# Kernel tuning notes

Hardware: AMD Instinct MI355X
Metric: run time of the kernel (lower is better)

Reference implementation:

```python
import jax, jax.numpy as jnp
import numpy as np

N, E, B = 65536, 262144, 2048   # nodes, edges, graphs
ND, ED, H, L = 32, 8, 128, 4    # node feat, edge feat, hidden, egnn layers
PE, PH, CH = 1280, 512, 512     # protein embed, protein hidden, combined hidden
EPS = 1e-8


def _seg_mean(data, ids, num):
    s = jax.ops.segment_sum(data, ids, num_segments=num)
    c = jax.ops.segment_sum(jnp.ones((data.shape[0], 1), data.dtype), ids, num_segments=num)
    return s / jnp.clip(c, 1.0)


def setup_inputs() -> dict:
    key = jax.random.key(0)
    ks = iter(jax.random.split(key, 40))

    def p(shape, scale=0.05):
        return jax.random.normal(next(ks), shape, dtype=jnp.float32) * scale

    inp = {
        "x": jax.random.normal(next(ks), (N, ND), dtype=jnp.float32),
        "pos": jax.random.normal(next(ks), (N, 3), dtype=jnp.float32),
        "edge_attr": jax.random.uniform(next(ks), (E, ED), dtype=jnp.float32),
        "protein_embedding": jax.random.normal(next(ks), (B, PE), dtype=jnp.float32),
        "edge_index": jax.random.randint(next(ks), (2, E), 0, N),
        "batch": jnp.arange(N, dtype=jnp.int64) // (N // B),
        # EGNN embeddings
        "emb_in_w": p((ND, H)), "emb_in_b": p((H,)),
        "emb_out_w": p((H, H)), "emb_out_b": p((H,)),
        # per-layer stacked params (leading dim L)
        "edge_w1": p((L, 2 * H + 1 + ED, H)), "edge_b1": p((L, H)),
        "edge_w2": p((L, H, H)), "edge_b2": p((L, H)),
        "att_w": p((L, H, 1)), "att_b": p((L, 1)),
        "coord_w1": p((L, H, H)), "coord_b1": p((L, H)),
        "coord_w2": p((L, H, 1)),  # no bias, xavier in torch impl
        "node_w1": p((L, 2 * H, H)), "node_b1": p((L, H)),
        "node_w2": p((L, H, H)), "node_b2": p((L, H)),
        # protein + combined heads
        "prot_w": p((PE, PH)), "prot_b": p((PH,)),
        "comb_w1": p((H + PH, CH)), "comb_b1": p((CH,)),
        "comb_w2": p((CH, 1)), "comb_b2": p((1,)),
    }
    return inp


def _forward(x, pos, edge_attr, protein_embedding,
             emb_in_w, emb_in_b, emb_out_w, emb_out_b,
             edge_w1, edge_b1, edge_w2, edge_b2, att_w, att_b,
             coord_w1, coord_b1, coord_w2,
             node_w1, node_b1, node_w2, node_b2,
             prot_w, prot_b, comb_w1, comb_b1, comb_w2, comb_b2,
             edge_index, batch):
    row, col = edge_index[0], edge_index[1]
    h = x @ emb_in_w + emb_in_b
    for l in range(L):
        # coord2radial (normalize=True)
        d = pos[row] - pos[col]                       # [E,3]
        radial = jnp.sum(d * d, axis=-1, keepdims=True)  # [E,1]
        d = d / (jnp.sqrt(radial) + EPS)
        # edge model with sigmoid attention gate
        e_in = jnp.concatenate([h[row], h[col], radial, edge_attr], axis=-1)
        m = jax.nn.silu(e_in @ edge_w1[l] + edge_b1[l])
        m = jax.nn.silu(m @ edge_w2[l] + edge_b2[l])
        m = m * jax.nn.sigmoid(m @ att_w[l] + att_b[l])
        # coord model (tanh=True, coords_agg='mean')
        t = jax.nn.silu(m @ coord_w1[l] + coord_b1[l])
        trans = d * jnp.tanh(t @ coord_w2[l])         # [E,3]
        pos = pos + _seg_mean(trans, row, N)
        # node model (sum aggregation, residual)
        agg = jax.ops.segment_sum(m, row, num_segments=N)
        nh = jax.nn.silu(jnp.concatenate([h, agg], axis=-1) @ node_w1[l] + node_b1[l])
        h = h + (nh @ node_w2[l] + node_b2[l])
    h = h @ emb_out_w + emb_out_b
    # global mean pool over graphs
    drug = _seg_mean(h, batch, B)                     # [B,H]
    prot = jax.nn.relu(protein_embedding @ prot_w + prot_b)  # dropout = identity (eval)
    c = jnp.concatenate([drug, prot], axis=-1)
    c = jax.nn.relu(c @ comb_w1 + comb_b1)
    logits = (c @ comb_w2 + comb_b2)[:, 0]
    return logits


def reference(x, pos, edge_attr, protein_embedding,
              emb_in_w, emb_in_b, emb_out_w, emb_out_b,
              edge_w1, edge_b1, edge_w2, edge_b2, att_w, att_b,
              coord_w1, coord_b1, coord_w2,
              node_w1, node_b1, node_w2, node_b2,
              prot_w, prot_b, comb_w1, comb_b1, comb_w2, comb_b2,
              edge_index, batch):
    logits = _forward(x, pos, edge_attr, protein_embedding,
                      emb_in_w, emb_in_b, emb_out_w, emb_out_b,
                      edge_w1, edge_b1, edge_w2, edge_b2, att_w, att_b,
                      coord_w1, coord_b1, coord_w2,
                      node_w1, node_b1, node_w2, node_b2,
                      prot_w, prot_b, comb_w1, comb_b1, comb_w2, comb_b2,
                      edge_index, batch)
    attention_weights = jnp.zeros((B, 1, 1), dtype=logits.dtype)
    return logits, attention_weights
```

## Files before the change

### kernel.cpp

```cpp
#include <hip/hip_runtime.h>
#include <math.h>


static constexpr int NN  = 65536;
static constexpr int NE  = 262144;
static constexpr int NB  = 2048;
static constexpr int NDF = 32;
static constexpr int HD  = 128;
static constexpr int NL  = 4;
static constexpr int PED = 1280;
static constexpr int PHD = 512;
static constexpr int CHD = 512;
static constexpr float EPSV = 1e-8f;

static constexpr int KK1 = 9;
static constexpr int KK2 = 4;
static constexpr int KKN1 = 8;
static constexpr int KKP = 40;
static constexpr int KKC = 20;

static constexpr int ES = 36;

typedef __attribute__((ext_vector_type(8))) short bf8_t;
typedef __attribute__((ext_vector_type(4))) float f4_t;

__device__ __forceinline__ float sigmoid_f(float x) {
  return __fdividef(1.0f, 1.0f + __expf(-x));
}
__device__ __forceinline__ float silu_f(float x) { return x * sigmoid_f(x); }

__device__ __forceinline__ ushort f2bf(float f) {
  unsigned u = __float_as_uint(f);
  u += 0x7FFFu + ((u >> 16) & 1u);
  return (ushort)(u >> 16);
}
__device__ __forceinline__ float bf2f(ushort h) {
  return __uint_as_float(((unsigned)h) << 16);
}
__device__ __forceinline__ unsigned pk2bf(float a, float b) {
  return (unsigned)f2bf(a) | ((unsigned)f2bf(b) << 16);
}

__device__ __forceinline__ void fma44(float (&acc)[4][4], const float4 a, const float4 w) {
  const float av[4] = {a.x, a.y, a.z, a.w};
  const float wv[4] = {w.x, w.y, w.z, w.w};
#pragma unroll
  for (int i = 0; i < 4; ++i)
#pragma unroll
    for (int j = 0; j < 4; ++j) acc[i][j] = fmaf(av[i], wv[j], acc[i][j]);
}


__global__ void hist_kernel(const int* __restrict__ ei, int* __restrict__ deg) {
  const int e = blockIdx.x * 256 + threadIdx.x;
  if (e < NE) atomicAdd(&deg[ei[e]], 1);
}

__global__ __launch_bounds__(1024) void scan_kernel(const int* __restrict__ deg,
                                                    int* __restrict__ row_ptr) {
  __shared__ int wsums[16];
  __shared__ int carry_s;
  const int t = threadIdx.x;
  const int lane = t & 63, wave = t >> 6;
  if (t == 0) { carry_s = 0; row_ptr[0] = 0; }
  __syncthreads();
  for (int c = 0; c < NN / 1024; ++c) {
    const int i = c * 1024 + t;
    int incl = deg[i];
#pragma unroll
    for (int d = 1; d < 64; d <<= 1) {
      const int u = __shfl_up(incl, d, 64);
      if (lane >= d) incl += u;
    }
    if (lane == 63) wsums[wave] = incl;
    __syncthreads();
    if (t == 0) {
      int a = carry_s;
#pragma unroll
      for (int w = 0; w < 16; ++w) { const int tmp = wsums[w]; wsums[w] = a; a += tmp; }
      carry_s = a;
    }
    __syncthreads();
    row_ptr[i + 1] = wsums[wave] + incl;
    __syncthreads();
  }
}

__global__ void fill_kernel(const int* __restrict__ ei, const int* __restrict__ row_ptr,
                            int* __restrict__ fill_pos, int* __restrict__ edge_ids) {
  const int e = blockIdx.x * 256 + threadIdx.x;
  if (e < NE) {
    const int n = ei[e];
    const int s = atomicAdd(&fill_pos[n], 1);
    edge_ids[row_ptr[n] + s] = e;
  }
}

__global__ void perm_kernel(const int* __restrict__ ei, const int* __restrict__ edge_ids,
                            const float* __restrict__ edge_attr,
                            int* __restrict__ rowp, int* __restrict__ colp,
                            float* __restrict__ eap) {
  const int i = blockIdx.x * 256 + threadIdx.x;
  if (i >= NE) return;
  const int e = edge_ids[i];
  rowp[i] = ei[e];
  colp[i] = ei[NE + e];
  const float4 a = *(const float4*)(edge_attr + (size_t)e * 8);
  const float4 b = *(const float4*)(edge_attr + (size_t)e * 8 + 4);
  *(float4*)(eap + (size_t)i * 8) = a;
  *(float4*)(eap + (size_t)i * 8 + 4) = b;
}

__global__ void pos_copy_kernel(const float* __restrict__ pos, float* __restrict__ pc) {
  const int n = blockIdx.x * 256 + threadIdx.x;
  if (n < NN) {
    const float4 v = make_float4(pos[(size_t)n * 3 + 0], pos[(size_t)n * 3 + 1],
                                 pos[(size_t)n * 3 + 2], 0.0f);
    *(float4*)(pc + (size_t)n * 4) = v;
  }
}


__global__ __launch_bounds__(256) void packw_kernel(
    const float* __restrict__ W, ushort* __restrict__ Wp,
    int K, int N, int KK, size_t sW, size_t sWp) {
  const int layer = blockIdx.y;
  const int NTG = N >> 4;
  const int i = blockIdx.x * 256 + threadIdx.x;
  if (i >= KK * NTG * 64) return;
  const int l = i & 63;
  const int q = i >> 6;
  const int ntg = q % NTG;
  const int kk = q / NTG;
  const int k0 = kk * 32 + ((l >> 4) * 8);
  const int n = ntg * 16 + (l & 15);
  const float* w = W + layer * sW;
  unsigned ww[4];
#pragma unroll
  for (int p = 0; p < 4; ++p) {
    const int ka = k0 + p * 2, kb = ka + 1;
    const unsigned lo = (ka < K) ? f2bf(w[(size_t)ka * N + n]) : 0;
    const unsigned hi = (kb < K) ? f2bf(w[(size_t)kb * N + n]) : 0;
    ww[p] = lo | (hi << 16);
  }
  *(uint4*)(Wp + layer * sWp + (size_t)i * 8) = make_uint4(ww[0], ww[1], ww[2], ww[3]);
}

__global__ __launch_bounds__(256) void cvt_bf_kernel(const float* __restrict__ in,
                                                     ushort* __restrict__ out, int n) {
  const int i = blockIdx.x * 256 + threadIdx.x;
  if (i * 8 >= n) return;
  const float4 v0 = *(const float4*)(in + (size_t)i * 8);
  const float4 v1 = *(const float4*)(in + (size_t)i * 8 + 4);
  *(uint4*)(out + (size_t)i * 8) =
      make_uint4(pk2bf(v0.x, v0.y), pk2bf(v0.z, v0.w), pk2bf(v1.x, v1.y), pk2bf(v1.z, v1.w));
}


__global__ __launch_bounds__(256) void geom_kernel(
    const float* __restrict__ pos_cur, const float* __restrict__ eap,
    const int* __restrict__ rowp, const int* __restrict__ colp,
    float* __restrict__ dnb, ushort* __restrict__ extra) {
  const int i = blockIdx.x * 256 + threadIdx.x;
  if (i >= NE) return;
  const int r = rowp[i], c = colp[i];
  const float4 pr = *(const float4*)(pos_cur + (size_t)r * 4);
  const float4 pc = *(const float4*)(pos_cur + (size_t)c * 4);
  const float dx = pr.x - pc.x, dy = pr.y - pc.y, dz = pr.z - pc.z;
  const float radial = dx * dx + dy * dy + dz * dz;
  const float inv = 1.0f / (sqrtf(radial) + EPSV);
  *(float4*)(dnb + (size_t)i * 4) = make_float4(dx * inv, dy * inv, dz * inv, 0.0f);
  const float4 ea0 = *(const float4*)(eap + (size_t)i * 8);
  const float4 ea1 = *(const float4*)(eap + (size_t)i * 8 + 4);
  ushort* dst = extra + (size_t)i * 32;
  *(uint4*)(dst) = make_uint4(pk2bf(radial, ea0.x), pk2bf(ea0.y, ea0.z),
                              pk2bf(ea0.w, ea1.x), pk2bf(ea1.y, ea1.z));
  *(uint4*)(dst + 8)  = make_uint4((unsigned)f2bf(ea1.w), 0, 0, 0);
  *(uint4*)(dst + 16) = make_uint4(0, 0, 0, 0);
  *(uint4*)(dst + 24) = make_uint4(0, 0, 0, 0);
}


__global__ __launch_bounds__(256) void emb_in_kernel(
    const float* __restrict__ x, const float* __restrict__ W,
    const float* __restrict__ B, float* __restrict__ h, ushort* __restrict__ hbf) {
  __shared__ float xs[NDF * ES];
  const int t = threadIdx.x;
  const int n0 = blockIdx.x * 32;
  {
    const int r = t >> 3;
    const int kq = (t & 7) * 4;
    const float4 v = *(const float4*)(x + (size_t)(n0 + r) * NDF + kq);
    xs[(kq + 0) * ES + r] = v.x;
    xs[(kq + 1) * ES + r] = v.y;
    xs[(kq + 2) * ES + r] = v.z;
    xs[(kq + 3) * ES + r] = v.w;
  }
  __syncthreads();
  const int eg = t & 7, fg = t >> 3;
  float acc[4][4] = {};
  const float* wp = W + fg * 4;
#pragma unroll
  for (int k = 0; k < NDF; ++k) {
    const float4 a = *(const float4*)&xs[k * ES + eg * 4];
    const float4 w = *(const float4*)(wp + (size_t)k * HD);
    fma44(acc, a, w);
  }
  const float4 bv = *(const float4*)(B + fg * 4);
  const float bb[4] = {bv.x, bv.y, bv.z, bv.w};
#pragma unroll
  for (int i = 0; i < 4; ++i) {
    const float4 o = make_float4(acc[i][0] + bb[0], acc[i][1] + bb[1],
                                 acc[i][2] + bb[2], acc[i][3] + bb[3]);
    *(float4*)(h + (size_t)(n0 + eg * 4 + i) * HD + fg * 4) = o;
    *(uint2*)(hbf + (size_t)(n0 + eg * 4 + i) * HD + fg * 4) =
        make_uint2(pk2bf(o.x, o.y), pk2bf(o.z, o.w));
  }
}


__global__ __launch_bounds__(256) void edge_mfma_kernel(
    const ushort* __restrict__ hbf, const ushort* __restrict__ extra,
    const int* __restrict__ rowp, const int* __restrict__ colp,
    const float* __restrict__ dnb,
    const ushort* __restrict__ W1p, const float* __restrict__ B1,
    const ushort* __restrict__ W2p, const float* __restrict__ B2,
    const float* __restrict__ AW, const float* __restrict__ AB,
    const ushort* __restrict__ CW1p, const float* __restrict__ CB1,
    const float* __restrict__ CW2,
    ushort* __restrict__ m_bf, float* __restrict__ trans_out) {
  __shared__ ushort mtileT[64 * 128];
  __shared__ int ridx[64], cidx[64];
  __shared__ float redbuf[2][64];
  __shared__ float gates[64];

  const int t = threadIdx.x;
  const int e0 = blockIdx.x * 64;
  if (t < 64) {
    ridx[t] = rowp[e0 + t];
    cidx[t] = colp[e0 + t];
  }
  __syncthreads();

  const int w = t >> 6, l = t & 63;
  const int wn = w & 1, we = w >> 1;
  const int g = l >> 4, ln = l & 15;
  const int nb = wn * 64;
  const int eb = we * 32;

  int je[2], er[2], ec[2], swz[2];
#pragma unroll
  for (int et = 0; et < 2; ++et) {
    je[et] = eb + et * 16 + ln;
    er[et] = ridx[je[et]];
    ec[et] = cidx[je[et]];
    swz[et] = (je[et] & 7) << 3;
  }

  const f4_t zf = {0.0f, 0.0f, 0.0f, 0.0f};
  f4_t acc[4][2];
#pragma unroll
  for (int mt = 0; mt < 4; ++mt)
#pragma unroll
    for (int et = 0; et < 2; ++et) acc[mt][et] = zf;

#pragma unroll
  for (int kk = 0; kk < KK1; ++kk) {
    bf8_t aw[4], be[2];
#pragma unroll
    for (int mt = 0; mt < 4; ++mt)
      aw[mt] = *(const bf8_t*)(W1p + ((size_t)(kk * 8 + wn * 4 + mt) * 64 + l) * 8);
#pragma unroll
    for (int et = 0; et < 2; ++et) {
      if (kk < 8) {
        const int idx = (kk < 4) ? er[et] : ec[et];
        be[et] = *(const bf8_t*)(hbf + (size_t)idx * HD + (kk & 3) * 32 + g * 8);
      } else {
        be[et] = *(const bf8_t*)(extra + (size_t)(e0 + je[et]) * 32 + g * 8);
      }
    }
#pragma unroll
    for (int mt = 0; mt < 4; ++mt)
#pragma unroll
      for (int et = 0; et < 2; ++et)
        acc[mt][et] = __builtin_amdgcn_mfma_f32_16x16x32_bf16(aw[mt], be[et], acc[mt][et], 0, 0, 0);
  }

  {
#pragma unroll
    for (int mt = 0; mt < 4; ++mt) {
      const int n0 = nb + mt * 16 + g * 4;
      const float4 bv = *(const float4*)(B1 + n0);
#pragma unroll
      for (int et = 0; et < 2; ++et) {
        const unsigned lo = pk2bf(silu_f(acc[mt][et][0] + bv.x), silu_f(acc[mt][et][1] + bv.y));
        const unsigned hi = pk2bf(silu_f(acc[mt][et][2] + bv.z), silu_f(acc[mt][et][3] + bv.w));
        *(uint2*)&mtileT[je[et] * HD + (n0 ^ swz[et])] = make_uint2(lo, hi);
      }
    }
  }
  __syncthreads();

  f4_t acc2[4][2];
#pragma unroll
  for (int mt = 0; mt < 4; ++mt)
#pragma unroll
    for (int et = 0; et < 2; ++et) acc2[mt][et] = zf;
#pragma unroll
  for (int kk = 0; kk < KK2; ++kk) {
    bf8_t aw[4], be[2];
#pragma unroll
    for (int mt = 0; mt < 4; ++mt)
      aw[mt] = *(const bf8_t*)(W2p + ((size_t)(kk * 8 + wn * 4 + mt) * 64 + l) * 8);
    const int nk = kk * 32 + g * 8;
#pragma unroll
    for (int et = 0; et < 2; ++et)
      be[et] = *(const bf8_t*)&mtileT[je[et] * HD + (nk ^ swz[et])];
#pragma unroll
    for (int mt = 0; mt < 4; ++mt)
#pragma unroll
      for (int et = 0; et < 2; ++et)
        acc2[mt][et] = __builtin_amdgcn_mfma_f32_16x16x32_bf16(aw[mt], be[et], acc2[mt][et], 0, 0, 0);
  }

  float m2v[4][2][4];
  {
    float p[2] = {0.0f, 0.0f};
#pragma unroll
    for (int mt = 0; mt < 4; ++mt) {
      const int n0 = nb + mt * 16 + g * 4;
      const float4 bv = *(const float4*)(B2 + n0);
      const float4 av = *(const float4*)(AW + n0);
      const float bb[4] = {bv.x, bv.y, bv.z, bv.w};
      const float aa[4] = {av.x, av.y, av.z, av.w};
#pragma unroll
      for (int et = 0; et < 2; ++et)
#pragma unroll
        for (int r = 0; r < 4; ++r) {
          const float v = silu_f(acc2[mt][et][r] + bb[r]);
          m2v[mt][et][r] = v;
          p[et] = fmaf(v, aa[r], p[et]);
        }
    }
#pragma unroll
    for (int et = 0; et < 2; ++et) {
      p[et] += __shfl_xor(p[et], 16, 64);
      p[et] += __shfl_xor(p[et], 32, 64);
    }
    if (l < 16) {
#pragma unroll
      for (int et = 0; et < 2; ++et) redbuf[wn][eb + et * 16 + l] = p[et];
    }
  }
  __syncthreads();
  if (t < 64) gates[t] = sigmoid_f(redbuf[0][t] + redbuf[1][t] + AB[0]);
  __syncthreads();

  {
    float grow[2];
#pragma unroll
    for (int et = 0; et < 2; ++et) grow[et] = gates[je[et]];
#pragma unroll
    for (int mt = 0; mt < 4; ++mt) {
      const int n0 = nb + mt * 16 + g * 4;
#pragma unroll
      for (int et = 0; et < 2; ++et) {
        const unsigned lo = pk2bf(m2v[mt][et][0] * grow[et], m2v[mt][et][1] * grow[et]);
        const unsigned hi = pk2bf(m2v[mt][et][2] * grow[et], m2v[mt][et][3] * grow[et]);
        *(uint2*)&mtileT[je[et] * HD + (n0 ^ swz[et])] = make_uint2(lo, hi);
      }
    }
  }
  __syncthreads();

  f4_t acc3[4][2];
#pragma unroll
  for (int mt = 0; mt < 4; ++mt)
#pragma unroll
    for (int et = 0; et < 2; ++et) acc3[mt][et] = zf;
#pragma unroll
  for (int kk = 0; kk < KK2; ++kk) {
    bf8_t aw[4], be[2];
#pragma unroll
    for (int mt = 0; mt < 4; ++mt)
      aw[mt] = *(const bf8_t*)(CW1p + ((size_t)(kk * 8 + wn * 4 + mt) * 64 + l) * 8);
    const int nk = kk * 32 + g * 8;
#pragma unroll
    for (int et = 0; et < 2; ++et)
      be[et] = *(const bf8_t*)&mtileT[je[et] * HD + (nk ^ swz[et])];
#pragma unroll
    for (int mt = 0; mt < 4; ++mt)
#pragma unroll
      for (int et = 0; et < 2; ++et)
        acc3[mt][et] = __builtin_amdgcn_mfma_f32_16x16x32_bf16(aw[mt], be[et], acc3[mt][et], 0, 0, 0);
  }
  {
    float q[2] = {0.0f, 0.0f};
#pragma unroll
    for (int mt = 0; mt < 4; ++mt) {
      const int n0 = nb + mt * 16 + g * 4;
      const float4 bv = *(const float4*)(CB1 + n0);
      const float4 cv = *(const float4*)(CW2 + n0);
      const float bb[4] = {bv.x, bv.y, bv.z, bv.w};
      const float cc[4] = {cv.x, cv.y, cv.z, cv.w};
#pragma unroll
      for (int et = 0; et < 2; ++et)
#pragma unroll
        for (int r = 0; r < 4; ++r)
          q[et] = fmaf(silu_f(acc3[mt][et][r] + bb[r]), cc[r], q[et]);
    }
#pragma unroll
    for (int et = 0; et < 2; ++et) {
      q[et] += __shfl_xor(q[et], 16, 64);
      q[et] += __shfl_xor(q[et], 32, 64);
    }
    if (l < 16) {
#pragma unroll
      for (int et = 0; et < 2; ++et) redbuf[wn][eb + et * 16 + l] = q[et];
    }
  }
  __syncthreads();
  if (t < 64) {
    const float s = tanhf(redbuf[0][t] + redbuf[1][t]);
    const f4_t dn = *(const f4_t*)(dnb + (size_t)(e0 + t) * 4);
    const f4_t tr = dn * s;
    *(f4_t*)(trans_out + (size_t)(e0 + t) * 4) = tr;
  }

#pragma unroll
  for (int it = 0; it < 4; ++it) {
    const int i = it * 256 + t;
    const int row = i >> 4;
    const int c8 = (i & 15) * 8;
    const uint4 v = *(const uint4*)&mtileT[row * HD + (c8 ^ ((row & 7) << 3))];
    *(uint4*)(m_bf + (size_t)(e0 + row) * HD + c8) = v;
  }
}


__global__ __launch_bounds__(256) void gather_kernel(
    const ushort* __restrict__ m_bf, const float* __restrict__ trans,
    const int* __restrict__ row_ptr,
    ushort* __restrict__ agg_bf, float* __restrict__ pos_cur) {
  const int t = threadIdx.x;
  const int wave = t >> 6, lane = t & 63;
  const int n = blockIdx.x * 4 + wave;
  const int s = row_ptr[n], e_end = row_ptr[n + 1];
  float a0 = 0.0f, a1 = 0.0f, ta = 0.0f;
  for (int i = s; i < e_end; ++i) {
    const ushort2 v = *(const ushort2*)(m_bf + (size_t)i * HD + lane * 2);
    a0 += bf2f(v.x);
    a1 += bf2f(v.y);
    if (lane < 4) ta += trans[(size_t)i * 4 + lane];
  }
  ushort2 ab;
  ab.x = f2bf(a0);
  ab.y = f2bf(a1);
  *(ushort2*)(agg_bf + (size_t)n * HD + lane * 2) = ab;
  if (lane < 3) {
    const int dg = e_end - s;
    pos_cur[(size_t)n * 4 + lane] += ta / (float)(dg > 0 ? dg : 1);
  }
}


__global__ __launch_bounds__(256) void node_mfma_kernel(
    float* __restrict__ h, const ushort* __restrict__ hbf,
    const ushort* __restrict__ agg_bf,
    const ushort* __restrict__ W1p, const float* __restrict__ B1,
    const ushort* __restrict__ W2p, const float* __restrict__ B2,
    ushort* __restrict__ hbf_out) {
  __shared__ ushort mtileT[64 * 128];
  const int t = threadIdx.x;
  const int n0blk = blockIdx.x * 64;
  const int w = t >> 6, l = t & 63;
  const int wn = w & 1, we = w >> 1;
  const int g = l >> 4, ln = l & 15;
  const int nb = wn * 64;
  const int eb = we * 32;

  int jn[2], swz[2];
#pragma unroll
  for (int et = 0; et < 2; ++et) {
    jn[et] = eb + et * 16 + ln;
    swz[et] = (jn[et] & 7) << 3;
  }

  const f4_t zf = {0.0f, 0.0f, 0.0f, 0.0f};
  f4_t acc[4][2];
#pragma unroll
  for (int mt = 0; mt < 4; ++mt)
#pragma unroll
    for (int et = 0; et < 2; ++et) acc[mt][et] = zf;

#pragma unroll
  for (int kk = 0; kk < KKN1; ++kk) {
    bf8_t aw[4], be[2];
#pragma unroll
    for (int mt = 0; mt < 4; ++mt)
      aw[mt] = *(const bf8_t*)(W1p + ((size_t)(kk * 8 + wn * 4 + mt) * 64 + l) * 8);
#pragma unroll
    for (int et = 0; et < 2; ++et) {
      const size_t base = (size_t)(n0blk + jn[et]) * HD + (kk & 3) * 32 + g * 8;
      be[et] = (kk < 4) ? *(const bf8_t*)(hbf + base) : *(const bf8_t*)(agg_bf + base);
    }
#pragma unroll
    for (int mt = 0; mt < 4; ++mt)
#pragma unroll
      for (int et = 0; et < 2; ++et)
        acc[mt][et] = __builtin_amdgcn_mfma_f32_16x16x32_bf16(aw[mt], be[et], acc[mt][et], 0, 0, 0);
  }
  {
#pragma unroll
    for (int mt = 0; mt < 4; ++mt) {
      const int n0 = nb + mt * 16 + g * 4;
      const float4 bv = *(const float4*)(B1 + n0);
#pragma unroll
      for (int et = 0; et < 2; ++et) {
        const unsigned lo = pk2bf(silu_f(acc[mt][et][0] + bv.x), silu_f(acc[mt][et][1] + bv.y));
        const unsigned hi = pk2bf(silu_f(acc[mt][et][2] + bv.z), silu_f(acc[mt][et][3] + bv.w));
        *(uint2*)&mtileT[jn[et] * HD + (n0 ^ swz[et])] = make_uint2(lo, hi);
      }
    }
  }
  __syncthreads();

  f4_t acc2[4][2];
#pragma unroll
  for (int mt = 0; mt < 4; ++mt)
#pragma unroll
    for (int et = 0; et < 2; ++et) acc2[mt][et] = zf;
#pragma unroll
  for (int kk = 0; kk < KK2; ++kk) {
    bf8_t aw[4], be[2];
#pragma unroll
    for (int mt = 0; mt < 4; ++mt)
      aw[mt] = *(const bf8_t*)(W2p + ((size_t)(kk * 8 + wn * 4 + mt) * 64 + l) * 8);
    const int nk = kk * 32 + g * 8;
#pragma unroll
    for (int et = 0; et < 2; ++et)
      be[et] = *(const bf8_t*)&mtileT[jn[et] * HD + (nk ^ swz[et])];
#pragma unroll
    for (int mt = 0; mt < 4; ++mt)
#pragma unroll
      for (int et = 0; et < 2; ++et)
        acc2[mt][et] = __builtin_amdgcn_mfma_f32_16x16x32_bf16(aw[mt], be[et], acc2[mt][et], 0, 0, 0);
  }
  {
#pragma unroll
    for (int mt = 0; mt < 4; ++mt) {
      const int n0 = nb + mt * 16 + g * 4;
      const float4 bv = *(const float4*)(B2 + n0);
#pragma unroll
      for (int et = 0; et < 2; ++et) {
        float* hp = h + (size_t)(n0blk + jn[et]) * HD + n0;
        const float4 old = *(const float4*)hp;
        float4 o;
        o.x = old.x + acc2[mt][et][0] + bv.x;
        o.y = old.y + acc2[mt][et][1] + bv.y;
        o.z = old.z + acc2[mt][et][2] + bv.z;
        o.w = old.w + acc2[mt][et][3] + bv.w;
        *(float4*)hp = o;
        *(uint2*)(hbf_out + (size_t)(n0blk + jn[et]) * HD + n0) =
            make_uint2(pk2bf(o.x, o.y), pk2bf(o.z, o.w));
      }
    }
  }
}


__global__ __launch_bounds__(256) void gemm_head_kernel(
    const ushort* __restrict__ A, const ushort* __restrict__ Wp,
    const float* __restrict__ bias, ushort* __restrict__ out,
    int lda, int KK, int NTG, int ldo, int col_off) {
  const int t = threadIdx.x;
  const int rb = blockIdx.x * 64;
  const int cb = blockIdx.y * 128;
  const int w = t >> 6, l = t & 63;
  const int wr = w >> 1, wc = w & 1;
  const int g = l >> 4, ln = l & 15;
  const int row0 = wr * 32;
  int rowA[2];
#pragma unroll
  for (int mt = 0; mt < 2; ++mt) rowA[mt] = row0 + mt * 16 + ln;

  const f4_t zf = {0.0f, 0.0f, 0.0f, 0.0f};
  f4_t acc[2][4];
#pragma unroll
  for (int mt = 0; mt < 2; ++mt)
#pragma unroll
    for (int nt = 0; nt < 4; ++nt) acc[mt][nt] = zf;

  const int ntg0 = (cb >> 4) + wc * 4;
  for (int kk = 0; kk < KK; ++kk) {
    bf8_t a[2], b[4];
#pragma unroll
    for (int mt = 0; mt < 2; ++mt)
      a[mt] = *(const bf8_t*)(A + (size_t)(rb + rowA[mt]) * lda + kk * 32 + g * 8);
#pragma unroll
    for (int nt = 0; nt < 4; ++nt)
      b[nt] = *(const bf8_t*)(Wp + ((size_t)(kk * NTG + ntg0 + nt) * 64 + l) * 8);
#pragma unroll
    for (int mt = 0; mt < 2; ++mt)
#pragma unroll
      for (int nt = 0; nt < 4; ++nt)
        acc[mt][nt] = __builtin_amdgcn_mfma_f32_16x16x32_bf16(a[mt], b[nt], acc[mt][nt], 0, 0, 0);
  }
  {
    float bn[4];
#pragma unroll
    for (int nt = 0; nt < 4; ++nt) bn[nt] = bias[cb + wc * 64 + nt * 16 + ln];
#pragma unroll
    for (int mt = 0; mt < 2; ++mt)
#pragma unroll
      for (int nt = 0; nt < 4; ++nt) {
        const int col = cb + wc * 64 + nt * 16 + ln;
#pragma unroll
        for (int r = 0; r < 4; ++r) {
          const int row = row0 + mt * 16 + g * 4 + r;
          const float v = fmaxf(acc[mt][nt][r] + bn[nt], 0.0f);
          out[(size_t)(rb + row) * ldo + col_off + col] = f2bf(v);
        }
      }
  }
}


__global__ __launch_bounds__(128) void pool_kernel(
    const float* __restrict__ h, const float* __restrict__ W,
    const float* __restrict__ B, ushort* __restrict__ c_in) {
  __shared__ float mh[HD];
  const int g = blockIdx.x, t = threadIdx.x;
  float s = 0.0f;
#pragma unroll 4
  for (int n = 0; n < 32; ++n) s += h[((size_t)g * 32 + n) * HD + t];
  mh[t] = s * (1.0f / 32.0f);
  __syncthreads();
  float acc = B[t];
#pragma unroll 4
  for (int k = 0; k < HD; ++k) acc = fmaf(mh[k], W[(size_t)k * HD + t], acc);
  c_in[(size_t)g * (HD + PHD) + t] = f2bf(acc);
}

__global__ __launch_bounds__(256) void logits_kernel(
    const ushort* __restrict__ c, const float* __restrict__ w2,
    const float* __restrict__ b2, float* __restrict__ out) {
  const int t = threadIdx.x;
  const int wave = t >> 6, lane = t & 63;
  const int r = blockIdx.x * 4 + wave;
  const ushort* cp = c + (size_t)r * CHD + lane * 8;
  const float* wp = w2 + lane * 8;
  float s = 0.0f;
#pragma unroll
  for (int j = 0; j < 8; ++j) s = fmaf(bf2f(cp[j]), wp[j], s);
#pragma unroll
  for (int off = 32; off > 0; off >>= 1) s += __shfl_down(s, off, 64);
  if (lane == 0) {
    out[r] = s + b2[0];
    out[NB + r] = 0.0f;
  }
}


extern "C" void kernel_launch(void* const* d_in, const int* in_sizes, int n_in,
                              void* d_out, int out_size, void* d_ws, size_t ws_size,
                              hipStream_t stream) {
  const float* x          = (const float*)d_in[0];
  const float* pos        = (const float*)d_in[1];
  const float* edge_attr  = (const float*)d_in[2];
  const float* pe         = (const float*)d_in[3];
  const int*   edge_index = (const int*)d_in[4];
  const float* emb_in_w   = (const float*)d_in[6];
  const float* emb_in_b   = (const float*)d_in[7];
  const float* emb_out_w  = (const float*)d_in[8];
  const float* emb_out_b  = (const float*)d_in[9];
  const float* edge_w1    = (const float*)d_in[10];
  const float* edge_b1    = (const float*)d_in[11];
  const float* edge_w2    = (const float*)d_in[12];
  const float* edge_b2    = (const float*)d_in[13];
  const float* att_w      = (const float*)d_in[14];
  const float* att_b      = (const float*)d_in[15];
  const float* coord_w1   = (const float*)d_in[16];
  const float* coord_b1   = (const float*)d_in[17];
  const float* coord_w2   = (const float*)d_in[18];
  const float* node_w1    = (const float*)d_in[19];
  const float* node_b1    = (const float*)d_in[20];
  const float* node_w2    = (const float*)d_in[21];
  const float* node_b2    = (const float*)d_in[22];
  const float* prot_w     = (const float*)d_in[23];
  const float* prot_b     = (const float*)d_in[24];
  const float* comb_w1    = (const float*)d_in[25];
  const float* comb_b1    = (const float*)d_in[26];
  const float* comb_w2    = (const float*)d_in[27];
  const float* comb_b2    = (const float*)d_in[28];
  float* out = (float*)d_out;
  (void)in_sizes; (void)n_in; (void)out_size; (void)ws_size;

  char* ws = (char*)d_ws;
  size_t off = 0;
  auto carve = [&](size_t bytes) -> void* {
    void* p = ws + off;
    off += (bytes + 255) & ~(size_t)255;
    return p;
  };
  float*  h       = (float*)carve((size_t)NN * HD * 4);
  ushort* h_bf    = (ushort*)carve((size_t)NN * HD * 2);
  ushort* agg_bf  = (ushort*)carve((size_t)NN * HD * 2);
  ushort* m_bf    = (ushort*)carve((size_t)NE * HD * 2);
  float*  trans   = (float*)carve((size_t)NE * 4 * 4);
  float*  dnb     = (float*)carve((size_t)NE * 4 * 4);
  ushort* extra   = (ushort*)carve((size_t)NE * 32 * 2);
  float*  eap     = (float*)carve((size_t)NE * 8 * 4);
  float*  pos_cur = (float*)carve((size_t)NN * 4 * 4);
  ushort* pe_bf   = (ushort*)carve((size_t)NB * PED * 2);
  ushort* c_in    = (ushort*)carve((size_t)NB * (HD + PHD) * 2);
  ushort* c1      = (ushort*)carve((size_t)NB * CHD * 2);
  const size_t sW1p  = (size_t)KK1 * 8 * 64 * 8;
  const size_t sW2p  = (size_t)KK2 * 8 * 64 * 8;
  const size_t sNW1p = (size_t)KKN1 * 8 * 64 * 8;
  const size_t sPWp  = (size_t)KKP * 32 * 64 * 8;
  const size_t sCWp  = (size_t)KKC * 32 * 64 * 8;
  ushort* W1p     = (ushort*)carve(sW1p * NL * 2);
  ushort* W2p     = (ushort*)carve(sW2p * NL * 2);
  ushort* CW1p    = (ushort*)carve(sW2p * NL * 2);
  ushort* NW1p    = (ushort*)carve(sNW1p * NL * 2);
  ushort* NW2p    = (ushort*)carve(sW2p * NL * 2);
  ushort* PWp     = (ushort*)carve(sPWp * 2);
  ushort* CWp     = (ushort*)carve(sCWp * 2);
  int* deg        = (int*)carve((size_t)NN * 4);
  int* row_ptr    = (int*)carve((size_t)(NN + 1) * 4);
  int* fill_pos   = (int*)carve((size_t)NN * 4);
  int* edge_ids   = (int*)carve((size_t)NE * 4);
  int* rowp       = (int*)carve((size_t)NE * 4);
  int* colp       = (int*)carve((size_t)NE * 4);

  hipMemsetAsync(deg, 0, (size_t)NN * 4, stream);
  hipMemsetAsync(fill_pos, 0, (size_t)NN * 4, stream);

  pos_copy_kernel<<<NN / 256, 256, 0, stream>>>(pos, pos_cur);
  hist_kernel<<<NE / 256, 256, 0, stream>>>(edge_index, deg);
  scan_kernel<<<1, 1024, 0, stream>>>(deg, row_ptr);
  fill_kernel<<<NE / 256, 256, 0, stream>>>(edge_index, row_ptr, fill_pos, edge_ids);
  perm_kernel<<<NE / 256, 256, 0, stream>>>(edge_index, edge_ids, edge_attr,
                                            rowp, colp, eap);

  packw_kernel<<<dim3(18, NL), 256, 0, stream>>>(edge_w1, W1p, 265, HD, KK1,
                                                 (size_t)265 * HD, sW1p);
  packw_kernel<<<dim3(8, NL), 256, 0, stream>>>(edge_w2, W2p, HD, HD, KK2,
                                                (size_t)HD * HD, sW2p);
  packw_kernel<<<dim3(8, NL), 256, 0, stream>>>(coord_w1, CW1p, HD, HD, KK2,
                                                (size_t)HD * HD, sW2p);
  packw_kernel<<<dim3(16, NL), 256, 0, stream>>>(node_w1, NW1p, 2 * HD, HD, KKN1,
                                                 (size_t)2 * HD * HD, sNW1p);
  packw_kernel<<<dim3(8, NL), 256, 0, stream>>>(node_w2, NW2p, HD, HD, KK2,
                                                (size_t)HD * HD, sW2p);
  packw_kernel<<<dim3(320, 1), 256, 0, stream>>>(prot_w, PWp, PED, PHD, KKP, 0, 0);
  packw_kernel<<<dim3(160, 1), 256, 0, stream>>>(comb_w1, CWp, HD + PHD, CHD, KKC, 0, 0);

  cvt_bf_kernel<<<NB * PED / (256 * 8), 256, 0, stream>>>(pe, pe_bf, NB * PED);

  emb_in_kernel<<<NN / 32, 256, 0, stream>>>(x, emb_in_w, emb_in_b, h, h_bf);

  for (int l = 0; l < NL; ++l) {
    geom_kernel<<<NE / 256, 256, 0, stream>>>(pos_cur, eap, rowp, colp, dnb, extra);
    edge_mfma_kernel<<<NE / 64, 256, 0, stream>>>(
        h_bf, extra, rowp, colp, dnb,
        W1p + (size_t)l * sW1p, edge_b1 + (size_t)l * HD,
        W2p + (size_t)l * sW2p, edge_b2 + (size_t)l * HD,
        att_w + (size_t)l * HD, att_b + l,
        CW1p + (size_t)l * sW2p, coord_b1 + (size_t)l * HD,
        coord_w2 + (size_t)l * HD,
        m_bf, trans);
    gather_kernel<<<NN / 4, 256, 0, stream>>>(m_bf, trans, row_ptr, agg_bf, pos_cur);
    node_mfma_kernel<<<NN / 64, 256, 0, stream>>>(
        h, h_bf, agg_bf,
        NW1p + (size_t)l * sNW1p, node_b1 + (size_t)l * HD,
        NW2p + (size_t)l * sW2p, node_b2 + (size_t)l * HD, h_bf);
  }

  pool_kernel<<<NB, 128, 0, stream>>>(h, emb_out_w, emb_out_b, c_in);
  gemm_head_kernel<<<dim3(NB / 64, PHD / 128), 256, 0, stream>>>(
      pe_bf, PWp, prot_b, c_in, PED, KKP, PHD / 16, HD + PHD, HD);
  gemm_head_kernel<<<dim3(NB / 64, CHD / 128), 256, 0, stream>>>(
      c_in, CWp, comb_b1, c1, HD + PHD, KKC, CHD / 16, CHD, 0);
  logits_kernel<<<NB / 4, 256, 0, stream>>>(c1, comb_w2, comb_b2, out);
}
```

Before: 1.026 ms.

## Enlarge edge/node MFMA tiles, parallelize scan, hoist edge-attr packing, use hw bf16 cvt

Edge and node MFMA kernels now process 128 rows per block instead of 64, so each wave computes a 4x4 accumulator tile and weight fragments are reused across more edges. Edge blocks are remapped in an interleaved order, and the second-layer activations are recomputed from the accumulators instead of being kept in registers. The single-block serial scan becomes a two-kernel parallel scan. Edge-attribute bf16 packing moves once into perm_kernel, so geom_kernel only writes the radial value, and pk2bf uses the hardware v_cvt_pk_bf16_f32 instruction. The larger tiles raise register and LDS pressure, which may reduce occupancy.

```diff
diff --git a/kernel.cpp b/kernel.cpp
--- a/kernel.cpp
+++ b/kernel.cpp
@@ -38,7 +38,9 @@
   return __uint_as_float(((unsigned)h) << 16);
 }
 __device__ __forceinline__ unsigned pk2bf(float a, float b) {
-  return (unsigned)f2bf(a) | ((unsigned)f2bf(b) << 16);
+  unsigned r;
+  asm("v_cvt_pk_bf16_f32 %0, %1, %2" : "=v"(r) : "v"(a), "v"(b));
+  return r;
 }
 
 __device__ __forceinline__ void fma44(float (&acc)[4][4], const float4 a, const float4 w) {
@@ -56,34 +58,51 @@
   if (e < NE) atomicAdd(&deg[ei[e]], 1);
 }
 
-__global__ __launch_bounds__(1024) void scan_kernel(const int* __restrict__ deg,
-                                                    int* __restrict__ row_ptr) {
-  __shared__ int wsums[16];
-  __shared__ int carry_s;
+__global__ __launch_bounds__(256) void scan1_kernel(const int* __restrict__ deg,
+                                                    int* __restrict__ cbase) {
+  __shared__ int wsum[4];
   const int t = threadIdx.x;
   const int lane = t & 63, wave = t >> 6;
-  if (t == 0) { carry_s = 0; row_ptr[0] = 0; }
-  __syncthreads();
-  for (int c = 0; c < NN / 1024; ++c) {
-    const int i = c * 1024 + t;
-    int incl = deg[i];
-#pragma unroll
-    for (int d = 1; d < 64; d <<= 1) {
-      const int u = __shfl_up(incl, d, 64);
-      if (lane >= d) incl += u;
-    }
-    if (lane == 63) wsums[wave] = incl;
-    __syncthreads();
-    if (t == 0) {
-      int a = carry_s;
-#pragma unroll
-      for (int w = 0; w < 16; ++w) { const int tmp = wsums[w]; wsums[w] = a; a += tmp; }
-      carry_s = a;
-    }
-    __syncthreads();
-    row_ptr[i + 1] = wsums[wave] + incl;
-    __syncthreads();
-  }
+  int s = 0;
+  const int4* p = (const int4*)deg + (size_t)t * 64;
+#pragma unroll 8
+  for (int j = 0; j < 64; ++j) {
+    const int4 v = p[j];
+    s += v.x + v.y + v.z + v.w;
+  }
+  int incl = s;
+#pragma unroll
+  for (int d = 1; d < 64; d <<= 1) {
+    const int u = __shfl_up(incl, d, 64);
+    if (lane >= d) incl += u;
+  }
+  if (lane == 63) wsum[wave] = incl;
+  __syncthreads();
+  int base = 0;
+  for (int w2 = 0; w2 < wave; ++w2) base += wsum[w2];
+  cbase[t] = base + incl - s;
+}
+
+__global__ __launch_bounds__(256) void scan2_kernel(const int* __restrict__ deg,
+                                                    const int* __restrict__ cbase,
+                                                    int* __restrict__ row_ptr) {
+  __shared__ int wsum[4];
+  const int b = blockIdx.x, t = threadIdx.x;
+  const int lane = t & 63, wave = t >> 6;
+  const int i = b * 256 + t;
+  const int s = deg[i];
+  int incl = s;
+#pragma unroll
+  for (int d = 1; d < 64; d <<= 1) {
+    const int u = __shfl_up(incl, d, 64);
+    if (lane >= d) incl += u;
+  }
+  if (lane == 63) wsum[wave] = incl;
+  __syncthreads();
+  int base = cbase[b];
+  for (int w2 = 0; w2 < wave; ++w2) base += wsum[w2];
+  row_ptr[i + 1] = base + incl;
+  if (i == 0) row_ptr[0] = 0;
 }
 
 __global__ void fill_kernel(const int* __restrict__ ei, const int* __restrict__ row_ptr,
@@ -99,7 +118,7 @@
 __global__ void perm_kernel(const int* __restrict__ ei, const int* __restrict__ edge_ids,
                             const float* __restrict__ edge_attr,
                             int* __restrict__ rowp, int* __restrict__ colp,
-                            float* __restrict__ eap) {
+                            ushort* __restrict__ extra) {
   const int i = blockIdx.x * 256 + threadIdx.x;
   if (i >= NE) return;
   const int e = edge_ids[i];
@@ -107,8 +126,12 @@
   colp[i] = ei[NE + e];
   const float4 a = *(const float4*)(edge_attr + (size_t)e * 8);
   const float4 b = *(const float4*)(edge_attr + (size_t)e * 8 + 4);
-  *(float4*)(eap + (size_t)i * 8) = a;
-  *(float4*)(eap + (size_t)i * 8 + 4) = b;
+  ushort* dst = extra + (size_t)i * 32;
+  *(uint4*)(dst) = make_uint4(pk2bf(0.0f, a.x), pk2bf(a.y, a.z),
+                              pk2bf(a.w, b.x), pk2bf(b.y, b.z));
+  *(uint4*)(dst + 8)  = make_uint4(pk2bf(b.w, 0.0f), 0, 0, 0);
+  *(uint4*)(dst + 16) = make_uint4(0, 0, 0, 0);
+  *(uint4*)(dst + 24) = make_uint4(0, 0, 0, 0);
 }
 
 __global__ void pos_copy_kernel(const float* __restrict__ pos, float* __restrict__ pc) {
@@ -158,7 +181,7 @@
 
 
 __global__ __launch_bounds__(256) void geom_kernel(
-    const float* __restrict__ pos_cur, const float* __restrict__ eap,
+    const float* __restrict__ pos_cur,
     const int* __restrict__ rowp, const int* __restrict__ colp,
     float* __restrict__ dnb, ushort* __restrict__ extra) {
   const int i = blockIdx.x * 256 + threadIdx.x;
@@ -170,14 +193,7 @@
   const float radial = dx * dx + dy * dy + dz * dz;
   const float inv = 1.0f / (sqrtf(radial) + EPSV);
   *(float4*)(dnb + (size_t)i * 4) = make_float4(dx * inv, dy * inv, dz * inv, 0.0f);
-  const float4 ea0 = *(const float4*)(eap + (size_t)i * 8);
-  const float4 ea1 = *(const float4*)(eap + (size_t)i * 8 + 4);
-  ushort* dst = extra + (size_t)i * 32;
-  *(uint4*)(dst) = make_uint4(pk2bf(radial, ea0.x), pk2bf(ea0.y, ea0.z),
-                              pk2bf(ea0.w, ea1.x), pk2bf(ea1.y, ea1.z));
-  *(uint4*)(dst + 8)  = make_uint4((unsigned)f2bf(ea1.w), 0, 0, 0);
-  *(uint4*)(dst + 16) = make_uint4(0, 0, 0, 0);
-  *(uint4*)(dst + 24) = make_uint4(0, 0, 0, 0);
+  extra[(size_t)i * 32] = f2bf(radial);
 }
 
 
@@ -229,14 +245,15 @@
     const ushort* __restrict__ CW1p, const float* __restrict__ CB1,
     const float* __restrict__ CW2,
     ushort* __restrict__ m_bf, float* __restrict__ trans_out) {
-  __shared__ ushort mtileT[64 * 128];
-  __shared__ int ridx[64], cidx[64];
-  __shared__ float redbuf[2][64];
-  __shared__ float gates[64];
+  __shared__ ushort mtileT[128 * 128];
+  __shared__ int ridx[128], cidx[128];
+  __shared__ float redbuf[2][128];
+  __shared__ float gates[128];
 
   const int t = threadIdx.x;
-  const int e0 = blockIdx.x * 64;
-  if (t < 64) {
+  const int bid = blockIdx.x;
+  const int e0 = ((bid & 7) * (NE / 128 / 8) + (bid >> 3)) * 128;
+  if (t < 128) {
     ridx[t] = rowp[e0 + t];
     cidx[t] = colp[e0 + t];
   }
@@ -246,11 +263,11 @@
   const int wn = w & 1, we = w >> 1;
   const int g = l >> 4, ln = l & 15;
   const int nb = wn * 64;
-  const int eb = we * 32;
-
-  int je[2], er[2], ec[2], swz[2];
-#pragma unroll
-  for (int et = 0; et < 2; ++et) {
+  const int eb = we * 64;
+
+  int je[4], er[4], ec[4], swz[4];
+#pragma unroll
+  for (int et = 0; et < 4; ++et) {
     je[et] = eb + et * 16 + ln;
     er[et] = ridx[je[et]];
     ec[et] = cidx[je[et]];
@@ -258,20 +275,20 @@
   }
 
   const f4_t zf = {0.0f, 0.0f, 0.0f, 0.0f};
-  f4_t acc[4][2];
+  f4_t acc[4][4];
 #pragma unroll
   for (int mt = 0; mt < 4; ++mt)
 #pragma unroll
-    for (int et = 0; et < 2; ++et) acc[mt][et] = zf;
+    for (int et = 0; et < 4; ++et) acc[mt][et] = zf;
 
 #pragma unroll
   for (int kk = 0; kk < KK1; ++kk) {
-    bf8_t aw[4], be[2];
+    bf8_t aw[4], be[4];
 #pragma unroll
     for (int mt = 0; mt < 4; ++mt)
       aw[mt] = *(const bf8_t*)(W1p + ((size_t)(kk * 8 + wn * 4 + mt) * 64 + l) * 8);
 #pragma unroll
-    for (int et = 0; et < 2; ++et) {
+    for (int et = 0; et < 4; ++et) {
       if (kk < 8) {
         const int idx = (kk < 4) ? er[et] : ec[et];
         be[et] = *(const bf8_t*)(hbf + (size_t)idx * HD + (kk & 3) * 32 + g * 8);
@@ -282,50 +299,47 @@
 #pragma unroll
     for (int mt = 0; mt < 4; ++mt)
 #pragma unroll
-      for (int et = 0; et < 2; ++et)
+      for (int et = 0; et < 4; ++et)
         acc[mt][et] = __builtin_amdgcn_mfma_f32_16x16x32_bf16(aw[mt], be[et], acc[mt][et], 0, 0, 0);
   }
 
-  {
-#pragma unroll
-    for (int mt = 0; mt < 4; ++mt) {
-      const int n0 = nb + mt * 16 + g * 4;
-      const float4 bv = *(const float4*)(B1 + n0);
-#pragma unroll
-      for (int et = 0; et < 2; ++et) {
-        const unsigned lo = pk2bf(silu_f(acc[mt][et][0] + bv.x), silu_f(acc[mt][et][1] + bv.y));
-        const unsigned hi = pk2bf(silu_f(acc[mt][et][2] + bv.z), silu_f(acc[mt][et][3] + bv.w));
-        *(uint2*)&mtileT[je[et] * HD + (n0 ^ swz[et])] = make_uint2(lo, hi);
-      }
-    }
-  }
-  __syncthreads();
-
-  f4_t acc2[4][2];
+#pragma unroll
+  for (int mt = 0; mt < 4; ++mt) {
+    const int n0 = nb + mt * 16 + g * 4;
+    const float4 bv = *(const float4*)(B1 + n0);
+#pragma unroll
+    for (int et = 0; et < 4; ++et) {
+      const unsigned lo = pk2bf(silu_f(acc[mt][et][0] + bv.x), silu_f(acc[mt][et][1] + bv.y));
+      const unsigned hi = pk2bf(silu_f(acc[mt][et][2] + bv.z), silu_f(acc[mt][et][3] + bv.w));
+      *(uint2*)&mtileT[je[et] * HD + (n0 ^ swz[et])] = make_uint2(lo, hi);
+    }
+  }
+  __syncthreads();
+
+  f4_t acc2[4][4];
 #pragma unroll
   for (int mt = 0; mt < 4; ++mt)
 #pragma unroll
-    for (int et = 0; et < 2; ++et) acc2[mt][et] = zf;
+    for (int et = 0; et < 4; ++et) acc2[mt][et] = zf;
 #pragma unroll
   for (int kk = 0; kk < KK2; ++kk) {
-    bf8_t aw[4], be[2];
+    bf8_t aw[4], be[4];
 #pragma unroll
     for (int mt = 0; mt < 4; ++mt)
       aw[mt] = *(const bf8_t*)(W2p + ((size_t)(kk * 8 + wn * 4 + mt) * 64 + l) * 8);
     const int nk = kk * 32 + g * 8;
 #pragma unroll
-    for (int et = 0; et < 2; ++et)
+    for (int et = 0; et < 4; ++et)
       be[et] = *(const bf8_t*)&mtileT[je[et] * HD + (nk ^ swz[et])];
 #pragma unroll
     for (int mt = 0; mt < 4; ++mt)
 #pragma unroll
-      for (int et = 0; et < 2; ++et)
+      for (int et = 0; et < 4; ++et)
         acc2[mt][et] = __builtin_amdgcn_mfma_f32_16x16x32_bf16(aw[mt], be[et], acc2[mt][et], 0, 0, 0);
   }
 
-  float m2v[4][2][4];
   {
-    float p[2] = {0.0f, 0.0f};
+    float p[4] = {0.0f, 0.0f, 0.0f, 0.0f};
 #pragma unroll
     for (int mt = 0; mt < 4; ++mt) {
       const int n0 = nb + mt * 16 + g * 4;
@@ -334,68 +348,64 @@
       const float bb[4] = {bv.x, bv.y, bv.z, bv.w};
       const float aa[4] = {av.x, av.y, av.z, av.w};
 #pragma unroll
-      for (int et = 0; et < 2; ++et)
-#pragma unroll
-        for (int r = 0; r < 4; ++r) {
-          const float v = silu_f(acc2[mt][et][r] + bb[r]);
-          m2v[mt][et][r] = v;
-          p[et] = fmaf(v, aa[r], p[et]);
-        }
-    }
-#pragma unroll
-    for (int et = 0; et < 2; ++et) {
+      for (int et = 0; et < 4; ++et)
+#pragma unroll
+        for (int r = 0; r < 4; ++r)
+          p[et] = fmaf(silu_f(acc2[mt][et][r] + bb[r]), aa[r], p[et]);
+    }
+#pragma unroll
+    for (int et = 0; et < 4; ++et) {
       p[et] += __shfl_xor(p[et], 16, 64);
       p[et] += __shfl_xor(p[et], 32, 64);
     }
     if (l < 16) {
 #pragma unroll
-      for (int et = 0; et < 2; ++et) redbuf[wn][eb + et * 16 + l] = p[et];
-    }
-  }
-  __syncthreads();
-  if (t < 64) gates[t] = sigmoid_f(redbuf[0][t] + redbuf[1][t] + AB[0]);
-  __syncthreads();
-
-  {
-    float grow[2];
-#pragma unroll
-    for (int et = 0; et < 2; ++et) grow[et] = gates[je[et]];
-#pragma unroll
-    for (int mt = 0; mt < 4; ++mt) {
-      const int n0 = nb + mt * 16 + g * 4;
-#pragma unroll
-      for (int et = 0; et < 2; ++et) {
-        const unsigned lo = pk2bf(m2v[mt][et][0] * grow[et], m2v[mt][et][1] * grow[et]);
-        const unsigned hi = pk2bf(m2v[mt][et][2] * grow[et], m2v[mt][et][3] * grow[et]);
-        *(uint2*)&mtileT[je[et] * HD + (n0 ^ swz[et])] = make_uint2(lo, hi);
-      }
-    }
-  }
-  __syncthreads();
-
-  f4_t acc3[4][2];
+      for (int et = 0; et < 4; ++et) redbuf[wn][eb + et * 16 + l] = p[et];
+    }
+  }
+  __syncthreads();
+  if (t < 128) gates[t] = sigmoid_f(redbuf[0][t] + redbuf[1][t] + AB[0]);
+  __syncthreads();
+
+#pragma unroll
+  for (int mt = 0; mt < 4; ++mt) {
+    const int n0 = nb + mt * 16 + g * 4;
+    const float4 bv = *(const float4*)(B2 + n0);
+#pragma unroll
+    for (int et = 0; et < 4; ++et) {
+      const float gr = gates[je[et]];
+      const unsigned lo = pk2bf(silu_f(acc2[mt][et][0] + bv.x) * gr,
+                                silu_f(acc2[mt][et][1] + bv.y) * gr);
+      const unsigned hi = pk2bf(silu_f(acc2[mt][et][2] + bv.z) * gr,
+                                silu_f(acc2[mt][et][3] + bv.w) * gr);
+      *(uint2*)&mtileT[je[et] * HD + (n0 ^ swz[et])] = make_uint2(lo, hi);
+    }
+  }
+  __syncthreads();
+
+  f4_t acc3[4][4];
 #pragma unroll
   for (int mt = 0; mt < 4; ++mt)
 #pragma unroll
-    for (int et = 0; et < 2; ++et) acc3[mt][et] = zf;
+    for (int et = 0; et < 4; ++et) acc3[mt][et] = zf;
 #pragma unroll
   for (int kk = 0; kk < KK2; ++kk) {
-    bf8_t aw[4], be[2];
+    bf8_t aw[4], be[4];
 #pragma unroll
     for (int mt = 0; mt < 4; ++mt)
       aw[mt] = *(const bf8_t*)(CW1p + ((size_t)(kk * 8 + wn * 4 + mt) * 64 + l) * 8);
     const int nk = kk * 32 + g * 8;
 #pragma unroll
-    for (int et = 0; et < 2; ++et)
+    for (int et = 0; et < 4; ++et)
       be[et] = *(const bf8_t*)&mtileT[je[et] * HD + (nk ^ swz[et])];
 #pragma unroll
     for (int mt = 0; mt < 4; ++mt)
 #pragma unroll
-      for (int et = 0; et < 2; ++et)
+      for (int et = 0; et < 4; ++et)
         acc3[mt][et] = __builtin_amdgcn_mfma_f32_16x16x32_bf16(aw[mt], be[et], acc3[mt][et], 0, 0, 0);
   }
   {
-    float q[2] = {0.0f, 0.0f};
+    float q[4] = {0.0f, 0.0f, 0.0f, 0.0f};
 #pragma unroll
     for (int mt = 0; mt < 4; ++mt) {
       const int n0 = nb + mt * 16 + g * 4;
@@ -404,23 +414,23 @@
       const float bb[4] = {bv.x, bv.y, bv.z, bv.w};
       const float cc[4] = {cv.x, cv.y, cv.z, cv.w};
 #pragma unroll
-      for (int et = 0; et < 2; ++et)
+      for (int et = 0; et < 4; ++et)
 #pragma unroll
         for (int r = 0; r < 4; ++r)
           q[et] = fmaf(silu_f(acc3[mt][et][r] + bb[r]), cc[r], q[et]);
     }
 #pragma unroll
-    for (int et = 0; et < 2; ++et) {
+    for (int et = 0; et < 4; ++et) {
       q[et] += __shfl_xor(q[et], 16, 64);
       q[et] += __shfl_xor(q[et], 32, 64);
     }
     if (l < 16) {
 #pragma unroll
-      for (int et = 0; et < 2; ++et) redbuf[wn][eb + et * 16 + l] = q[et];
-    }
-  }
-  __syncthreads();
-  if (t < 64) {
+      for (int et = 0; et < 4; ++et) redbuf[wn][eb + et * 16 + l] = q[et];
+    }
+  }
+  __syncthreads();
+  if (t < 128) {
     const float s = tanhf(redbuf[0][t] + redbuf[1][t]);
     const f4_t dn = *(const f4_t*)(dnb + (size_t)(e0 + t) * 4);
     const f4_t tr = dn * s;
@@ -428,7 +438,7 @@
   }
 
 #pragma unroll
-  for (int it = 0; it < 4; ++it) {
+  for (int it = 0; it < 8; ++it) {
     const int i = it * 256 + t;
     const int row = i >> 4;
     const int c8 = (i & 15) * 8;
@@ -453,10 +463,7 @@
     a1 += bf2f(v.y);
     if (lane < 4) ta += trans[(size_t)i * 4 + lane];
   }
-  ushort2 ab;
-  ab.x = f2bf(a0);
-  ab.y = f2bf(a1);
-  *(ushort2*)(agg_bf + (size_t)n * HD + lane * 2) = ab;
+  *(unsigned*)(agg_bf + (size_t)n * HD + lane * 2) = pk2bf(a0, a1);
   if (lane < 3) {
     const int dg = e_end - s;
     pos_cur[(size_t)n * 4 + lane] += ta / (float)(dg > 0 ? dg : 1);
@@ -470,100 +477,96 @@
     const ushort* __restrict__ W1p, const float* __restrict__ B1,
     const ushort* __restrict__ W2p, const float* __restrict__ B2,
     ushort* __restrict__ hbf_out) {
-  __shared__ ushort mtileT[64 * 128];
+  __shared__ ushort mtileT[128 * 128];
   const int t = threadIdx.x;
-  const int n0blk = blockIdx.x * 64;
+  const int n0blk = blockIdx.x * 128;
   const int w = t >> 6, l = t & 63;
   const int wn = w & 1, we = w >> 1;
   const int g = l >> 4, ln = l & 15;
   const int nb = wn * 64;
-  const int eb = we * 32;
-
-  int jn[2], swz[2];
-#pragma unroll
-  for (int et = 0; et < 2; ++et) {
+  const int eb = we * 64;
+
+  int jn[4], swz[4];
+#pragma unroll
+  for (int et = 0; et < 4; ++et) {
     jn[et] = eb + et * 16 + ln;
     swz[et] = (jn[et] & 7) << 3;
   }
 
   const f4_t zf = {0.0f, 0.0f, 0.0f, 0.0f};
-  f4_t acc[4][2];
+  f4_t acc[4][4];
 #pragma unroll
   for (int mt = 0; mt < 4; ++mt)
 #pragma unroll
-    for (int et = 0; et < 2; ++et) acc[mt][et] = zf;
+    for (int et = 0; et < 4; ++et) acc[mt][et] = zf;
 
 #pragma unroll
   for (int kk = 0; kk < KKN1; ++kk) {
-    bf8_t aw[4], be[2];
+    bf8_t aw[4], be[4];
 #pragma unroll
     for (int mt = 0; mt < 4; ++mt)
       aw[mt] = *(const bf8_t*)(W1p + ((size_t)(kk * 8 + wn * 4 + mt) * 64 + l) * 8);
 #pragma unroll
-    for (int et = 0; et < 2; ++et) {
+    for (int et = 0; et < 4; ++et) {
       const size_t base = (size_t)(n0blk + jn[et]) * HD + (kk & 3) * 32 + g * 8;
       be[et] = (kk < 4) ? *(const bf8_t*)(hbf + base) : *(const bf8_t*)(agg_bf + base);
     }
 #pragma unroll
     for (int mt = 0; mt < 4; ++mt)
 #pragma unroll
-      for (int et = 0; et < 2; ++et)
+      for (int et = 0; et < 4; ++et)
         acc[mt][et] = __builtin_amdgcn_mfma_f32_16x16x32_bf16(aw[mt], be[et], acc[mt][et], 0, 0, 0);
   }
-  {
-#pragma unroll
-    for (int mt = 0; mt < 4; ++mt) {
-      const int n0 = nb + mt * 16 + g * 4;
-      const float4 bv = *(const float4*)(B1 + n0);
-#pragma unroll
-      for (int et = 0; et < 2; ++et) {
-        const unsigned lo = pk2bf(silu_f(acc[mt][et][0] + bv.x), silu_f(acc[mt][et][1] + bv.y));
-        const unsigned hi = pk2bf(silu_f(acc[mt][et][2] + bv.z), silu_f(acc[mt][et][3] + bv.w));
-        *(uint2*)&mtileT[jn[et] * HD + (n0 ^ swz[et])] = make_uint2(lo, hi);
-      }
-    }
-  }
-  __syncthreads();
-
-  f4_t acc2[4][2];
+#pragma unroll
+  for (int mt = 0; mt < 4; ++mt) {
+    const int n0 = nb + mt * 16 + g * 4;
+    const float4 bv = *(const float4*)(B1 + n0);
+#pragma unroll
+    for (int et = 0; et < 4; ++et) {
+      const unsigned lo = pk2bf(silu_f(acc[mt][et][0] + bv.x), silu_f(acc[mt][et][1] + bv.y));
+      const unsigned hi = pk2bf(silu_f(acc[mt][et][2] + bv.z), silu_f(acc[mt][et][3] + bv.w));
+      *(uint2*)&mtileT[jn[et] * HD + (n0 ^ swz[et])] = make_uint2(lo, hi);
+    }
+  }
+  __syncthreads();
+
+  f4_t acc2[4][4];
 #pragma unroll
   for (int mt = 0; mt < 4; ++mt)
 #pragma unroll
-    for (int et = 0; et < 2; ++et) acc2[mt][et] = zf;
+    for (int et = 0; et < 4; ++et) acc2[mt][et] = zf;
 #pragma unroll
   for (int kk = 0; kk < KK2; ++kk) {
-    bf8_t aw[4], be[2];
+    bf8_t aw[4], be[4];
 #pragma unroll
     for (int mt = 0; mt < 4; ++mt)
       aw[mt] = *(const bf8_t*)(W2p + ((size_t)(kk * 8 + wn * 4 + mt) * 64 + l) * 8);
     const int nk = kk * 32 + g * 8;
 #pragma unroll
-    for (int et = 0; et < 2; ++et)
+    for (int et = 0; et < 4; ++et)
       be[et] = *(const bf8_t*)&mtileT[jn[et] * HD + (nk ^ swz[et])];
 #pragma unroll
     for (int mt = 0; mt < 4; ++mt)
 #pragma unroll
-      for (int et = 0; et < 2; ++et)
+      for (int et = 0; et < 4; ++et)
         acc2[mt][et] = __builtin_amdgcn_mfma_f32_16x16x32_bf16(aw[mt], be[et], acc2[mt][et], 0, 0, 0);
   }
-  {
-#pragma unroll
-    for (int mt = 0; mt < 4; ++mt) {
-      const int n0 = nb + mt * 16 + g * 4;
-      const float4 bv = *(const float4*)(B2 + n0);
-#pragma unroll
-      for (int et = 0; et < 2; ++et) {
-        float* hp = h + (size_t)(n0blk + jn[et]) * HD + n0;
-        const float4 old = *(const float4*)hp;
-        float4 o;
-        o.x = old.x + acc2[mt][et][0] + bv.x;
-        o.y = old.y + acc2[mt][et][1] + bv.y;
-        o.z = old.z + acc2[mt][et][2] + bv.z;
-        o.w = old.w + acc2[mt][et][3] + bv.w;
-        *(float4*)hp = o;
-        *(uint2*)(hbf_out + (size_t)(n0blk + jn[et]) * HD + n0) =
-            make_uint2(pk2bf(o.x, o.y), pk2bf(o.z, o.w));
-      }
+#pragma unroll
+  for (int mt = 0; mt < 4; ++mt) {
+    const int n0 = nb + mt * 16 + g * 4;
+    const float4 bv = *(const float4*)(B2 + n0);
+#pragma unroll
+    for (int et = 0; et < 4; ++et) {
+      float* hp = h + (size_t)(n0blk + jn[et]) * HD + n0;
+      const float4 old = *(const float4*)hp;
+      float4 o;
+      o.x = old.x + acc2[mt][et][0] + bv.x;
+      o.y = old.y + acc2[mt][et][1] + bv.y;
+      o.z = old.z + acc2[mt][et][2] + bv.z;
+      o.w = old.w + acc2[mt][et][3] + bv.w;
+      *(float4*)hp = o;
+      *(uint2*)(hbf_out + (size_t)(n0blk + jn[et]) * HD + n0) =
+          make_uint2(pk2bf(o.x, o.y), pk2bf(o.z, o.w));
     }
   }
 }
@@ -710,7 +713,6 @@
   float*  trans   = (float*)carve((size_t)NE * 4 * 4);
   float*  dnb     = (float*)carve((size_t)NE * 4 * 4);
   ushort* extra   = (ushort*)carve((size_t)NE * 32 * 2);
-  float*  eap     = (float*)carve((size_t)NE * 8 * 4);
   float*  pos_cur = (float*)carve((size_t)NN * 4 * 4);
   ushort* pe_bf   = (ushort*)carve((size_t)NB * PED * 2);
   ushort* c_in    = (ushort*)carve((size_t)NB * (HD + PHD) * 2);
@@ -733,16 +735,18 @@
   int* edge_ids   = (int*)carve((size_t)NE * 4);
   int* rowp       = (int*)carve((size_t)NE * 4);
   int* colp       = (int*)carve((size_t)NE * 4);
+  int* cbase      = (int*)carve((size_t)256 * 4);
 
   hipMemsetAsync(deg, 0, (size_t)NN * 4, stream);
   hipMemsetAsync(fill_pos, 0, (size_t)NN * 4, stream);
 
   pos_copy_kernel<<<NN / 256, 256, 0, stream>>>(pos, pos_cur);
   hist_kernel<<<NE / 256, 256, 0, stream>>>(edge_index, deg);
-  scan_kernel<<<1, 1024, 0, stream>>>(deg, row_ptr);
+  scan1_kernel<<<1, 256, 0, stream>>>(deg, cbase);
+  scan2_kernel<<<NN / 256, 256, 0, stream>>>(deg, cbase, row_ptr);
   fill_kernel<<<NE / 256, 256, 0, stream>>>(edge_index, row_ptr, fill_pos, edge_ids);
   perm_kernel<<<NE / 256, 256, 0, stream>>>(edge_index, edge_ids, edge_attr,
-                                            rowp, colp, eap);
+                                            rowp, colp, extra);
 
   packw_kernel<<<dim3(18, NL), 256, 0, stream>>>(edge_w1, W1p, 265, HD, KK1,
                                                  (size_t)265 * HD, sW1p);
@@ -762,8 +766,8 @@
   emb_in_kernel<<<NN / 32, 256, 0, stream>>>(x, emb_in_w, emb_in_b, h, h_bf);
 
   for (int l = 0; l < NL; ++l) {
-    geom_kernel<<<NE / 256, 256, 0, stream>>>(pos_cur, eap, rowp, colp, dnb, extra);
-    edge_mfma_kernel<<<NE / 64, 256, 0, stream>>>(
+    geom_kernel<<<NE / 256, 256, 0, stream>>>(pos_cur, rowp, colp, dnb, extra);
+    edge_mfma_kernel<<<NE / 128, 256, 0, stream>>>(
         h_bf, extra, rowp, colp, dnb,
         W1p + (size_t)l * sW1p, edge_b1 + (size_t)l * HD,
         W2p + (size_t)l * sW2p, edge_b2 + (size_t)l * HD,
@@ -772,7 +776,7 @@
         coord_w2 + (size_t)l * HD,
         m_bf, trans);
     gather_kernel<<<NN / 4, 256, 0, stream>>>(m_bf, trans, row_ptr, agg_bf, pos_cur);
-    node_mfma_kernel<<<NN / 64, 256, 0, stream>>>(
+    node_mfma_kernel<<<NN / 128, 256, 0, stream>>>(
         h, h_bf, agg_bf,
         NW1p + (size_t)l * sNW1p, node_b1 + (size_t)l * HD,
         NW2p + (size_t)l * sW2p, node_b2 + (size_t)l * HD, h_bf);
```

Result: slower. 1.189 ms (+15.9%).
